# Performance work log

Measured on AMD Instinct MI355X. Metric: run time of the kernel, lower is better.

Reference implementation:

```python
import jax, jax.numpy as jnp
import numpy as np

TAU = 20.0        # LIFNeuron default tau
THRESHOLD = 1.0   # LIFNeuron default threshold
RESET = 0.0       # LIFNeuron default reset
DT = 1.0          # SpikingNeuralNetwork dt
ALPHA = DT / TAU

B, T, I, H, O = 256, 128, 512, 1024, 512


def setup_inputs() -> dict:
    key = jax.random.key(0)
    ks = jax.random.split(key, 6)
    def w(k, shape, fan_in):
        return (jax.random.normal(k, shape, jnp.float32) / np.sqrt(fan_in)).astype(jnp.float32)
    return {
        "x":  jax.random.normal(ks[0], (B, T, I), jnp.float32),
        "We": w(ks[1], (I, H), I), "be": jnp.zeros((H,), jnp.float32),
        "W1": w(ks[2], (H, H), H), "b1": jnp.zeros((H,), jnp.float32),
        "W2": w(ks[3], (H, H), H), "b2": jnp.zeros((H,), jnp.float32),
        "Wo": w(ks[4], (H, O), H), "bo": jnp.zeros((O,), jnp.float32),
    }


def _lif(v, inp):
    # v += (-v + inp) * dt/tau; spike = (v >= thr); v = v*(1-spike) + reset*spike
    v = v + (inp - v) * ALPHA
    spike = (v >= THRESHOLD).astype(v.dtype)
    v = v * (1.0 - spike) + RESET * spike
    return v, spike


def reference(x, We, be, W1, b1, W2, b2, Wo, bo):
    b, t, _ = x.shape
    h_dim = We.shape[1]
    o_dim = Wo.shape[1]

    def step(carry, xt):
        v1, v2, vo = carry
        h = jax.nn.relu(xt @ We + be)          # [B, H]
        v1, s1 = _lif(v1, h)                   # neuron 0 (only 2 of 3 neurons used: zip truncation)
        h = s1 @ W1 + b1
        v2, s2 = _lif(v2, h)                   # neuron 1
        h = s2 @ W2 + b2                       # last hidden layer: no neuron applied before output_layer
        vo, so = _lif(vo, h @ Wo + bo)         # output neuron
        return (v1, v2, vo), (s1, s2, so)

    init = (jnp.zeros((b, h_dim), x.dtype),
            jnp.zeros((b, h_dim), x.dtype),
            jnp.zeros((b, o_dim), x.dtype))
    _, (S1, S2, SO) = jax.lax.scan(step, init, jnp.swapaxes(x, 0, 1))  # time-major scan
    # output_spike at last timestep + full (detached) spike history, stacked over time
    return SO[-1], S1, S2, SO
```

## Files before the change

kernel.cpp:

```cpp
#include <hip/hip_runtime.h>
#include <cstdint>
#include <cstddef>

#define B_ 256
#define T_ 128
#define I_ 512
#define H_ 1024
#define O_ 512
static constexpr float ALPHA = 1.0f / 20.0f;
static constexpr float THR   = 1.0f;
static constexpr float S12   = 0.000244140625f;

typedef _Float16 f16;
typedef __attribute__((ext_vector_type(8))) _Float16 f16x8;
typedef __attribute__((ext_vector_type(4))) float f32x4;

template<bool PERM_X, bool RELU>
__global__ __launch_bounds__(256)
void gemm128(const float* __restrict__ A, const float* __restrict__ Bw,
             const float* __restrict__ bias, float* __restrict__ C,
             int M, int N, int K) {
    constexpr int BM = 128, BN = 128, BK = 16, TM = 8, TN = 8;
    __shared__ float As[BK][BM];
    __shared__ float Bs[BK][BN + 4];

    const int tid = threadIdx.x;
    const int ntile = N / BN;
    const int bx = blockIdx.x % ntile;
    const int by = blockIdx.x / ntile;
    const int row0 = by * BM, col0 = bx * BN;
    const int tx = tid & 15;
    const int ty = tid >> 4;

    float acc[TM][TN] = {};

    for (int k0 = 0; k0 < K; k0 += BK) {
#pragma unroll
        for (int p = 0; p < 2; ++p) {
            int f = tid + p * 256;
            int r  = f >> 2;
            int kc = (f & 3) << 2;
            int m = row0 + r;
            const float* arow;
            if (PERM_X) {
                int t = m >> 8;
                int b = m & 255;
                arow = A + (size_t)(b * T_ + t) * K;
            } else {
                arow = A + (size_t)m * K;
            }
            float4 v = *reinterpret_cast<const float4*>(arow + k0 + kc);
            As[kc + 0][r] = v.x;
            As[kc + 1][r] = v.y;
            As[kc + 2][r] = v.z;
            As[kc + 3][r] = v.w;
        }
#pragma unroll
        for (int p = 0; p < 2; ++p) {
            int f = tid + p * 256;
            int r  = f >> 5;
            int nc = (f & 31) << 2;
            float4 v = *reinterpret_cast<const float4*>(Bw + (size_t)(k0 + r) * N + col0 + nc);
            *reinterpret_cast<float4*>(&Bs[r][nc]) = v;
        }
        __syncthreads();

#pragma unroll
        for (int k = 0; k < BK; ++k) {
            float a[TM], b[TN];
#pragma unroll
            for (int i = 0; i < TM; ++i) a[i] = As[k][ty * TM + i];
#pragma unroll
            for (int j = 0; j < TN; ++j) b[j] = Bs[k][tx * TN + j];
#pragma unroll
            for (int i = 0; i < TM; ++i)
#pragma unroll
                for (int j = 0; j < TN; ++j)
                    acc[i][j] += a[i] * b[j];
        }
        __syncthreads();
    }

#pragma unroll
    for (int i = 0; i < TM; ++i) {
        size_t m = (size_t)(row0 + ty * TM + i);
#pragma unroll
        for (int jj = 0; jj < TN; jj += 4) {
            int n = col0 + tx * TN + jj;
            float4 c4;
            float c0 = acc[i][jj + 0] + bias[n + 0];
            float c1 = acc[i][jj + 1] + bias[n + 1];
            float c2 = acc[i][jj + 2] + bias[n + 2];
            float c3 = acc[i][jj + 3] + bias[n + 3];
            if (RELU) {
                c0 = fmaxf(c0, 0.f); c1 = fmaxf(c1, 0.f);
                c2 = fmaxf(c2, 0.f); c3 = fmaxf(c3, 0.f);
            }
            c4.x = c0; c4.y = c1; c4.z = c2; c4.w = c3;
            *reinterpret_cast<float4*>(C + m * N + n) = c4;
        }
    }
}

__device__ inline void gload_lds16(const void* gsrc, void* ldsdst) {
    __builtin_amdgcn_global_load_lds(
        (const __attribute__((address_space(1))) unsigned int*)gsrc,
        (__attribute__((address_space(3))) unsigned int*)ldsdst, 16, 0, 0);
}

template<bool SPLITX, bool PERM, bool RELU, bool WRITE_LAST>
__global__ __launch_bounds__(256, 2)
void gemm_lif(const float* __restrict__ A,
              const f16* __restrict__ Bhi,
              const f16* __restrict__ Blo,
              const float* __restrict__ bias,
              float* __restrict__ S,
              float* __restrict__ last_out,
              int N, int K) {
    constexpr int BK = 32;
    __shared__ __align__(16) char smem[128 * 132 * 4];
    f16* Ah = (f16*)smem;
    f16* Bh = Ah + 4096;
    f16* Bl = Bh + 4096;
    f16* Al = Bl + 4096;
    float (*Cs)[132] = (float (*)[132])smem;

    const int tid  = threadIdx.x;
    const int lane = tid & 63;
    const int w    = tid >> 6;
    const int wr   = w >> 1, wc = w & 1;
    const int ntile = N >> 7;
    const int bx = blockIdx.x % ntile;
    const int b  = blockIdx.x / ntile;
    const int col0 = bx << 7;

    f32x4 acc0[4][4], acc1[4][4];
#pragma unroll
    for (int mi = 0; mi < 4; ++mi)
#pragma unroll
        for (int ni = 0; ni < 4; ++ni) {
            acc0[mi][ni] = {0.f, 0.f, 0.f, 0.f};
            acc1[mi][ni] = {0.f, 0.f, 0.f, 0.f};
        }

    for (int k0 = 0; k0 < K; k0 += BK) {
#pragma unroll
        for (int p = 0; p < 2; ++p) {
            int chunk = w * 2 + p;
            int r  = chunk * 16 + (lane >> 2);
            int kq = lane & 3;
            size_t off = (size_t)(col0 + r) * K + k0 + kq * 8;
            gload_lds16(Bhi + off, &Bh[chunk * 512]);
            gload_lds16(Blo + off, &Bl[chunk * 512]);
        }
#pragma unroll
        for (int p = 0; p < 4; ++p) {
            int c = tid + p * 256;
            int r = c >> 3;
            int q = c & 7;
            const float* arow;
            if (PERM) arow = A + (size_t)(b * T_ + r) * K;
            else      arow = A + (size_t)(r * B_ + b) * K;
            float4 v = *reinterpret_cast<const float4*>(arow + k0 + q * 4);
            union { f16 h[4]; uint2 u; } hi;
            hi.h[0] = (f16)v.x; hi.h[1] = (f16)v.y;
            hi.h[2] = (f16)v.z; hi.h[3] = (f16)v.w;
            *reinterpret_cast<uint2*>(&Ah[r * BK + q * 4]) = hi.u;
            if (SPLITX) {
                union { f16 h[4]; uint2 u; } lo;
                lo.h[0] = (f16)((v.x - (float)hi.h[0]) * 4096.0f);
                lo.h[1] = (f16)((v.y - (float)hi.h[1]) * 4096.0f);
                lo.h[2] = (f16)((v.z - (float)hi.h[2]) * 4096.0f);
                lo.h[3] = (f16)((v.w - (float)hi.h[3]) * 4096.0f);
                *reinterpret_cast<uint2*>(&Al[r * BK + q * 4]) = lo.u;
            }
        }
        __syncthreads();

        f16x8 ahi[4], alo[4];
#pragma unroll
        for (int mi = 0; mi < 4; ++mi) {
            int ar = (wr * 64 + mi * 16 + (lane & 15)) * BK + (lane >> 4) * 8;
            ahi[mi] = *reinterpret_cast<const f16x8*>(&Ah[ar]);
            if (SPLITX) alo[mi] = *reinterpret_cast<const f16x8*>(&Al[ar]);
        }
#pragma unroll
        for (int ni = 0; ni < 4; ++ni) {
            int br = (wc * 64 + ni * 16 + (lane & 15)) * BK + (lane >> 4) * 8;
            f16x8 bh = *reinterpret_cast<const f16x8*>(&Bh[br]);
            f16x8 bl = *reinterpret_cast<const f16x8*>(&Bl[br]);
#pragma unroll
            for (int mi = 0; mi < 4; ++mi) {
                acc0[mi][ni] = __builtin_amdgcn_mfma_f32_16x16x32_f16(
                    ahi[mi], bh, acc0[mi][ni], 0, 0, 0);
                acc1[mi][ni] = __builtin_amdgcn_mfma_f32_16x16x32_f16(
                    ahi[mi], bl, acc1[mi][ni], 0, 0, 0);
                if (SPLITX)
                    acc1[mi][ni] = __builtin_amdgcn_mfma_f32_16x16x32_f16(
                        alo[mi], bh, acc1[mi][ni], 0, 0, 0);
            }
        }
        __syncthreads();
    }

#pragma unroll
    for (int ni = 0; ni < 4; ++ni) {
        int col = wc * 64 + ni * 16 + (lane & 15);
        float bv = bias[col0 + col];
#pragma unroll
        for (int mi = 0; mi < 4; ++mi) {
            int rowb = wr * 64 + mi * 16 + ((lane >> 4) << 2);
#pragma unroll
            for (int r = 0; r < 4; ++r) {
                float cv = acc0[mi][ni][r] + S12 * acc1[mi][ni][r] + bv;
                if (RELU) cv = fmaxf(cv, 0.f);
                Cs[rowb + r][col] = cv;
            }
        }
    }
    __syncthreads();

    if (tid < 128) {
        float* Sp = S + (size_t)b * N + col0 + tid;
        const size_t tstride = (size_t)B_ * N;
        float v = 0.f, s = 0.f;
#pragma unroll 4
        for (int t = 0; t < T_; ++t) {
            float in = Cs[t][tid];
            v = v + (in - v) * ALPHA;
            bool sp = (v >= THR);
            s = sp ? 1.0f : 0.0f;
            Sp[(size_t)t * tstride] = s;
            v = sp ? 0.0f : v;
        }
        if (WRITE_LAST) last_out[(size_t)b * N + col0 + tid] = s;
    }
}

__global__ __launch_bounds__(256)
void lif_scan(float* __restrict__ buf, int BH, float* __restrict__ last_out) {
    int j = blockIdx.x * 256 + threadIdx.x;
    if (j >= BH) return;
    float v = 0.f;
    float last = 0.f;
    for (int t = 0; t < T_; ++t) {
        size_t idx = (size_t)t * BH + j;
        float in = buf[idx];
        v = v + (in - v) * ALPHA;
        bool sp = (v >= THR);
        last = sp ? 1.0f : 0.0f;
        buf[idx] = last;
        v = sp ? 0.0f : v;
    }
    if (last_out) last_out[j] = last;
}

__global__ __launch_bounds__(256)
void make_wf2(const float* __restrict__ W2, const float* __restrict__ Wo,
              float* __restrict__ Wf) {
    __shared__ float w2s[64][33];
    __shared__ float wos[64][68];
    const int tid = threadIdx.x;
    const int ht = blockIdx.x >> 3, ot = blockIdx.x & 7;
    const int h0 = ht * 32, o0 = ot * 64;
    const int th = tid >> 3;
    const int to = tid & 7;

    double acc[8] = {0, 0, 0, 0, 0, 0, 0, 0};

    for (int k0 = 0; k0 < H_; k0 += 64) {
#pragma unroll
        for (int p = 0; p < 2; ++p) {
            int f = tid + p * 256;
            int i = f >> 4;
            int j4 = (f & 15) << 2;
            float4 v = *reinterpret_cast<const float4*>(
                W2 + (size_t)(h0 + i) * H_ + k0 + j4);
            w2s[j4 + 0][i] = v.x; w2s[j4 + 1][i] = v.y;
            w2s[j4 + 2][i] = v.z; w2s[j4 + 3][i] = v.w;
        }
#pragma unroll
        for (int p = 0; p < 4; ++p) {
            int f = tid + p * 256;
            int r = f >> 4;
            int c4 = (f & 15) << 2;
            float4 v = *reinterpret_cast<const float4*>(
                Wo + (size_t)(k0 + r) * O_ + o0 + c4);
            wos[r][c4 + 0] = v.x; wos[r][c4 + 1] = v.y;
            wos[r][c4 + 2] = v.z; wos[r][c4 + 3] = v.w;
        }
        __syncthreads();

#pragma unroll 8
        for (int k = 0; k < 64; ++k) {
            double a = (double)w2s[k][th];
#pragma unroll
            for (int j = 0; j < 8; ++j)
                acc[j] += a * (double)wos[k][to * 8 + j];
        }
        __syncthreads();
    }
#pragma unroll
    for (int j = 0; j < 8; ++j)
        Wf[(size_t)(h0 + th) * O_ + o0 + to * 8 + j] = (float)acc[j];
}

__global__ __launch_bounds__(256)
void make_bf(const float* __restrict__ Wo, const float* __restrict__ b2,
             const float* __restrict__ bo, float* __restrict__ bf) {
    int o = blockIdx.x * 256 + threadIdx.x;
    if (o >= O_) return;
    double acc = (double)bo[o];
    for (int h = 0; h < H_; ++h)
        acc += (double)b2[h] * (double)Wo[(size_t)h * O_ + o];
    bf[o] = (float)acc;
}

__global__ __launch_bounds__(256)
void split_w16(const float* __restrict__ W, f16* __restrict__ hi,
               f16* __restrict__ lo, int K, int N) {
    int idx = blockIdx.x * 256 + threadIdx.x;
    if (idx >= K * N) return;
    int n = idx / K;
    int k = idx - n * K;
    float wv = W[(size_t)k * N + n];
    f16 h0 = (f16)wv;
    float r = (wv - (float)h0) * 4096.0f;
    f16 h1 = (f16)r;
    hi[idx] = h0; lo[idx] = h1;
}

extern "C" void kernel_launch(void* const* d_in, const int* in_sizes, int n_in,
                              void* d_out, int out_size, void* d_ws, size_t ws_size,
                              hipStream_t stream) {
    const float* x  = (const float*)d_in[0];
    const float* We = (const float*)d_in[1];
    const float* be = (const float*)d_in[2];
    const float* W1 = (const float*)d_in[3];
    const float* b1 = (const float*)d_in[4];
    const float* W2 = (const float*)d_in[5];
    const float* b2 = (const float*)d_in[6];
    const float* Wo = (const float*)d_in[7];
    const float* bo = (const float*)d_in[8];

    float* out = (float*)d_out;
    float* so_last = out;
    float* S1 = out + (size_t)B_ * O_;
    float* S2 = S1 + (size_t)T_ * B_ * H_;
    float* SO = S2 + (size_t)T_ * B_ * H_;

    const int TB = T_ * B_;
    dim3 blk(256);

    const size_t sz_we  = (size_t)I_ * H_ * 2;
    const size_t sz_w1  = (size_t)H_ * H_ * 2;
    const size_t sz_wf  = (size_t)H_ * O_ * 2;
    const size_t off_weh = 0;
    const size_t off_wel = off_weh + sz_we;
    const size_t off_w1h = off_wel + sz_we;
    const size_t off_w1l = off_w1h + sz_w1;
    const size_t off_wf32 = off_w1l + sz_w1;
    const size_t off_bf   = off_wf32 + (size_t)H_ * O_ * 4;
    const size_t off_wfh  = off_bf + (size_t)O_ * 4;
    const size_t off_wfl  = off_wfh + sz_wf;
    const size_t need     = off_wfl + sz_wf;

    if (ws_size >= need) {
        char* ws = (char*)d_ws;
        f16*   weh = (f16*)(ws + off_weh);
        f16*   wel = (f16*)(ws + off_wel);
        f16*   w1h = (f16*)(ws + off_w1h);
        f16*   w1l = (f16*)(ws + off_w1l);
        float* Wf  = (float*)(ws + off_wf32);
        float* bf  = (float*)(ws + off_bf);
        f16*   wfh = (f16*)(ws + off_wfh);
        f16*   wfl = (f16*)(ws + off_wfl);

        split_w16<<<dim3((I_ * H_ + 255) / 256), blk, 0, stream>>>(We, weh, wel, I_, H_);
        split_w16<<<dim3((H_ * H_ + 255) / 256), blk, 0, stream>>>(W1, w1h, w1l, H_, H_);
        make_wf2<<<dim3(256), blk, 0, stream>>>(W2, Wo, Wf);
        make_bf<<<dim3(2), blk, 0, stream>>>(Wo, b2, bo, bf);
        split_w16<<<dim3((H_ * O_ + 255) / 256), blk, 0, stream>>>(Wf, wfh, wfl, H_, O_);

        gemm_lif<true, true, true, false><<<dim3(B_ * (H_ / 128)), blk, 0, stream>>>(
            x, weh, wel, be, S1, nullptr, H_, I_);

        gemm_lif<false, false, false, false><<<dim3(B_ * (H_ / 128)), blk, 0, stream>>>(
            S1, w1h, w1l, b1, S2, nullptr, H_, H_);

        gemm_lif<false, false, false, true><<<dim3(B_ * (O_ / 128)), blk, 0, stream>>>(
            S2, wfh, wfl, bf, SO, so_last, O_, H_);
    } else {
        float* Wf = (float*)d_ws;
        float* bf = Wf + (size_t)H_ * O_;
        gemm128<true, true><<<dim3((TB / 128) * (H_ / 128)), blk, 0, stream>>>(
            x, We, be, S1, TB, H_, I_);
        lif_scan<<<dim3((B_ * H_ + 255) / 256), blk, 0, stream>>>(S1, B_ * H_, nullptr);
        gemm128<false, false><<<dim3((TB / 128) * (H_ / 128)), blk, 0, stream>>>(
            S1, W1, b1, S2, TB, H_, H_);
        lif_scan<<<dim3((B_ * H_ + 255) / 256), blk, 0, stream>>>(S2, B_ * H_, nullptr);
        make_wf2<<<dim3(256), blk, 0, stream>>>(W2, Wo, Wf);
        make_bf<<<dim3(2), blk, 0, stream>>>(Wo, b2, bo, bf);
        gemm128<false, false><<<dim3((TB / 128) * (O_ / 128)), blk, 0, stream>>>(
            S2, Wf, bf, SO, TB, O_, H_);
        lif_scan<<<dim3((B_ * O_ + 255) / 256), blk, 0, stream>>>(SO, B_ * O_, so_last);
    }
}
```

Before: 643.4 us.

## Use 512-thread blocks, halve LDS epilogue with two-phase LIF scan, reorder grid

The fused GEMM+LIF kernel now runs with 512 threads (8 waves in a 2x4 layout), so each wave holds half the accumulators. The C staging buffer is cut to 64 rows, and the epilogue writes and scans the two halves of the time axis in turn. Together these lower LDS and register use so more blocks can be resident per CU. The block index now puts the batch in the low bits, so consecutive blocks share a weight column tile, which may improve L2 reuse of weights. The cost is extra barriers, and only 128 threads are busy during the serial LIF scan while the other waves sit idle.

After: 699.8 us. 8.8% more time.

```diff
diff --git a/kernel.cpp b/kernel.cpp
--- a/kernel.cpp
+++ b/kernel.cpp
@@ -109,7 +109,7 @@
 }
 
 template<bool SPLITX, bool PERM, bool RELU, bool WRITE_LAST>
-__global__ __launch_bounds__(256, 2)
+__global__ __launch_bounds__(512, 4)
 void gemm_lif(const float* __restrict__ A,
               const f16* __restrict__ Bhi,
               const f16* __restrict__ Blo,
@@ -118,7 +118,7 @@
               float* __restrict__ last_out,
               int N, int K) {
     constexpr int BK = 32;
-    __shared__ __align__(16) char smem[128 * 132 * 4];
+    __shared__ __align__(16) char smem[64 * 132 * 4];
     f16* Ah = (f16*)smem;
     f16* Bh = Ah + 4096;
     f16* Bl = Bh + 4096;
@@ -128,34 +128,32 @@
     const int tid  = threadIdx.x;
     const int lane = tid & 63;
     const int w    = tid >> 6;
-    const int wr   = w >> 1, wc = w & 1;
-    const int ntile = N >> 7;
-    const int bx = blockIdx.x % ntile;
-    const int b  = blockIdx.x / ntile;
+    const int wr   = w >> 2;
+    const int wc   = w & 3;
+    const int b    = blockIdx.x & 255;
+    const int bx   = blockIdx.x >> 8;
     const int col0 = bx << 7;
 
-    f32x4 acc0[4][4], acc1[4][4];
+    f32x4 acc0[4][2], acc1[4][2];
 #pragma unroll
     for (int mi = 0; mi < 4; ++mi)
 #pragma unroll
-        for (int ni = 0; ni < 4; ++ni) {
+        for (int ni = 0; ni < 2; ++ni) {
             acc0[mi][ni] = {0.f, 0.f, 0.f, 0.f};
             acc1[mi][ni] = {0.f, 0.f, 0.f, 0.f};
         }
 
     for (int k0 = 0; k0 < K; k0 += BK) {
-#pragma unroll
-        for (int p = 0; p < 2; ++p) {
-            int chunk = w * 2 + p;
-            int r  = chunk * 16 + (lane >> 2);
+        {
+            int r  = w * 16 + (lane >> 2);
             int kq = lane & 3;
             size_t off = (size_t)(col0 + r) * K + k0 + kq * 8;
-            gload_lds16(Bhi + off, &Bh[chunk * 512]);
-            gload_lds16(Blo + off, &Bl[chunk * 512]);
-        }
-#pragma unroll
-        for (int p = 0; p < 4; ++p) {
-            int c = tid + p * 256;
+            gload_lds16(Bhi + off, &Bh[w * 512]);
+            gload_lds16(Blo + off, &Bl[w * 512]);
+        }
+#pragma unroll
+        for (int p = 0; p < 2; ++p) {
+            int c = tid + p * 512;
             int r = c >> 3;
             int q = c & 7;
             const float* arow;
@@ -185,8 +183,8 @@
             if (SPLITX) alo[mi] = *reinterpret_cast<const f16x8*>(&Al[ar]);
         }
 #pragma unroll
-        for (int ni = 0; ni < 4; ++ni) {
-            int br = (wc * 64 + ni * 16 + (lane & 15)) * BK + (lane >> 4) * 8;
+        for (int ni = 0; ni < 2; ++ni) {
+            int br = (wc * 32 + ni * 16 + (lane & 15)) * BK + (lane >> 4) * 8;
             f16x8 bh = *reinterpret_cast<const f16x8*>(&Bh[br]);
             f16x8 bl = *reinterpret_cast<const f16x8*>(&Bl[br]);
 #pragma unroll
@@ -203,30 +201,62 @@
         __syncthreads();
     }
 
-#pragma unroll
-    for (int ni = 0; ni < 4; ++ni) {
-        int col = wc * 64 + ni * 16 + (lane & 15);
-        float bv = bias[col0 + col];
-#pragma unroll
-        for (int mi = 0; mi < 4; ++mi) {
-            int rowb = wr * 64 + mi * 16 + ((lane >> 4) << 2);
-#pragma unroll
-            for (int r = 0; r < 4; ++r) {
-                float cv = acc0[mi][ni][r] + S12 * acc1[mi][ni][r] + bv;
-                if (RELU) cv = fmaxf(cv, 0.f);
-                Cs[rowb + r][col] = cv;
+    float v = 0.f, s = 0.f;
+    float* Sp = S + (size_t)b * N + col0 + (tid & 127);
+    const size_t tstride = (size_t)B_ * N;
+
+    if (wr == 0) {
+#pragma unroll
+        for (int ni = 0; ni < 2; ++ni) {
+            int col = wc * 32 + ni * 16 + (lane & 15);
+            float bv = bias[col0 + col];
+#pragma unroll
+            for (int mi = 0; mi < 4; ++mi) {
+                int rowb = mi * 16 + ((lane >> 4) << 2);
+#pragma unroll
+                for (int r = 0; r < 4; ++r) {
+                    float cv = acc0[mi][ni][r] + S12 * acc1[mi][ni][r] + bv;
+                    if (RELU) cv = fmaxf(cv, 0.f);
+                    Cs[rowb + r][col] = cv;
+                }
             }
         }
     }
     __syncthreads();
-
     if (tid < 128) {
-        float* Sp = S + (size_t)b * N + col0 + tid;
-        const size_t tstride = (size_t)B_ * N;
-        float v = 0.f, s = 0.f;
 #pragma unroll 4
-        for (int t = 0; t < T_; ++t) {
+        for (int t = 0; t < 64; ++t) {
             float in = Cs[t][tid];
+            v = v + (in - v) * ALPHA;
+            bool sp = (v >= THR);
+            s = sp ? 1.0f : 0.0f;
+            Sp[(size_t)t * tstride] = s;
+            v = sp ? 0.0f : v;
+        }
+    }
+    __syncthreads();
+    if (wr == 1) {
+#pragma unroll
+        for (int ni = 0; ni < 2; ++ni) {
+            int col = wc * 32 + ni * 16 + (lane & 15);
+            float bv = bias[col0 + col];
+#pragma unroll
+            for (int mi = 0; mi < 4; ++mi) {
+                int rowb = mi * 16 + ((lane >> 4) << 2);
+#pragma unroll
+                for (int r = 0; r < 4; ++r) {
+                    float cv = acc0[mi][ni][r] + S12 * acc1[mi][ni][r] + bv;
+                    if (RELU) cv = fmaxf(cv, 0.f);
+                    Cs[rowb + r][col] = cv;
+                }
+            }
+        }
+    }
+    __syncthreads();
+    if (tid < 128) {
+#pragma unroll 4
+        for (int t = 64; t < 128; ++t) {
+            float in = Cs[t - 64][tid];
             v = v + (in - v) * ALPHA;
             bool sp = (v >= THR);
             s = sp ? 1.0f : 0.0f;
@@ -351,6 +381,7 @@
 
     const int TB = T_ * B_;
     dim3 blk(256);
+    dim3 blk512(512);
 
     const size_t sz_we  = (size_t)I_ * H_ * 2;
     const size_t sz_w1  = (size_t)H_ * H_ * 2;
@@ -382,13 +413,13 @@
         make_bf<<<dim3(2), blk, 0, stream>>>(Wo, b2, bo, bf);
         split_w16<<<dim3((H_ * O_ + 255) / 256), blk, 0, stream>>>(Wf, wfh, wfl, H_, O_);
 
-        gemm_lif<true, true, true, false><<<dim3(B_ * (H_ / 128)), blk, 0, stream>>>(
+        gemm_lif<true, true, true, false><<<dim3((H_ / 128) * B_), blk512, 0, stream>>>(
             x, weh, wel, be, S1, nullptr, H_, I_);
 
-        gemm_lif<false, false, false, false><<<dim3(B_ * (H_ / 128)), blk, 0, stream>>>(
+        gemm_lif<false, false, false, false><<<dim3((H_ / 128) * B_), blk512, 0, stream>>>(
             S1, w1h, w1l, b1, S2, nullptr, H_, H_);
 
-        gemm_lif<false, false, false, true><<<dim3(B_ * (O_ / 128)), blk, 0, stream>>>(
+        gemm_lif<false, false, false, true><<<dim3((O_ / 128) * B_), blk512, 0, stream>>>(
             S2, wfh, wfl, bf, SO, so_last, O_, H_);
     } else {
         float* Wf = (float*)d_ws;
```

## Double-buffer LDS tiles in fused GEMM+LIF and split epilogue into halves

Applied to the files above, without the earlier changes.

Adds double buffering to the gemm_lif main loop. The next K-tile's B halves are issued via global_load_lds and its A rows are prefetched into registers while MFMAs run on the current tile, leaving one barrier per iteration instead of two. To keep the LDS footprint bounded, the epilogue now stages the 128x128 result in two 64-row halves, with the LIF time scan run over each half in turn. This costs more LDS for the two buffers, extra barriers in the epilogue, and more register pressure from the prefetched float4s, which may hurt occupancy at launch_bounds(256,2).

Result: no change. 644.3 us (+0.1%).

```diff
diff --git a/kernel.cpp b/kernel.cpp
--- a/kernel.cpp
+++ b/kernel.cpp
@@ -118,11 +118,13 @@
               float* __restrict__ last_out,
               int N, int K) {
     constexpr int BK = 32;
-    __shared__ __align__(16) char smem[128 * 132 * 4];
-    f16* Ah = (f16*)smem;
-    f16* Bh = Ah + 4096;
-    f16* Bl = Bh + 4096;
-    f16* Al = Bl + 4096;
+    constexpr int NBUF = SPLITX ? 4 : 3;
+    constexpr int BUFSTR = NBUF * 4096;
+    constexpr size_t SMEM = (2 * BUFSTR * 2 > 64 * 132 * 4)
+                                ? (size_t)(2 * BUFSTR * 2)
+                                : (size_t)(64 * 132 * 4);
+    __shared__ __align__(16) char smem[SMEM];
+    f16* sm = (f16*)smem;
     float (*Cs)[132] = (float (*)[132])smem;
 
     const int tid  = threadIdx.x;
@@ -143,90 +145,187 @@
             acc1[mi][ni] = {0.f, 0.f, 0.f, 0.f};
         }
 
-    for (int k0 = 0; k0 < K; k0 += BK) {
+    {
+        f16* Ah0 = sm;
+        f16* Bh0 = sm + 4096;
+        f16* Bl0 = sm + 8192;
+        f16* Al0 = sm + 12288;
 #pragma unroll
         for (int p = 0; p < 2; ++p) {
             int chunk = w * 2 + p;
             int r  = chunk * 16 + (lane >> 2);
             int kq = lane & 3;
-            size_t off = (size_t)(col0 + r) * K + k0 + kq * 8;
-            gload_lds16(Bhi + off, &Bh[chunk * 512]);
-            gload_lds16(Blo + off, &Bl[chunk * 512]);
+            size_t off = (size_t)(col0 + r) * K + kq * 8;
+            gload_lds16(Bhi + off, Bh0 + chunk * 512);
+            gload_lds16(Blo + off, Bl0 + chunk * 512);
         }
 #pragma unroll
         for (int p = 0; p < 4; ++p) {
             int c = tid + p * 256;
             int r = c >> 3;
             int q = c & 7;
-            const float* arow;
-            if (PERM) arow = A + (size_t)(b * T_ + r) * K;
-            else      arow = A + (size_t)(r * B_ + b) * K;
-            float4 v = *reinterpret_cast<const float4*>(arow + k0 + q * 4);
+            const float* arow = PERM ? A + (size_t)(b * T_ + r) * K
+                                     : A + (size_t)(r * B_ + b) * K;
+            float4 v = *reinterpret_cast<const float4*>(arow + q * 4);
             union { f16 h[4]; uint2 u; } hi;
             hi.h[0] = (f16)v.x; hi.h[1] = (f16)v.y;
             hi.h[2] = (f16)v.z; hi.h[3] = (f16)v.w;
-            *reinterpret_cast<uint2*>(&Ah[r * BK + q * 4]) = hi.u;
+            *reinterpret_cast<uint2*>(&Ah0[r * BK + q * 4]) = hi.u;
             if (SPLITX) {
                 union { f16 h[4]; uint2 u; } lo;
                 lo.h[0] = (f16)((v.x - (float)hi.h[0]) * 4096.0f);
                 lo.h[1] = (f16)((v.y - (float)hi.h[1]) * 4096.0f);
                 lo.h[2] = (f16)((v.z - (float)hi.h[2]) * 4096.0f);
                 lo.h[3] = (f16)((v.w - (float)hi.h[3]) * 4096.0f);
-                *reinterpret_cast<uint2*>(&Al[r * BK + q * 4]) = lo.u;
+                *reinterpret_cast<uint2*>(&Al0[r * BK + q * 4]) = lo.u;
+            }
+        }
+    }
+    __syncthreads();
+
+    const int NIT = K / BK;
+    for (int it = 0; it < NIT; ++it) {
+        const int cur = it & 1, nxt = cur ^ 1;
+        const bool more = (it + 1 < NIT);
+        const int k0n = (it + 1) * BK;
+
+        f16* Ah_c = sm + cur * BUFSTR;
+        f16* Bh_c = Ah_c + 4096;
+        f16* Bl_c = Ah_c + 8192;
+        f16* Al_c = Ah_c + 12288;
+        f16* Ah_n = sm + nxt * BUFSTR;
+        f16* Bh_n = Ah_n + 4096;
+        f16* Bl_n = Ah_n + 8192;
+        f16* Al_n = Ah_n + 12288;
+
+        float4 a4[4];
+        if (more) {
+#pragma unroll
+            for (int p = 0; p < 2; ++p) {
+                int chunk = w * 2 + p;
+                int r  = chunk * 16 + (lane >> 2);
+                int kq = lane & 3;
+                size_t off = (size_t)(col0 + r) * K + k0n + kq * 8;
+                gload_lds16(Bhi + off, Bh_n + chunk * 512);
+                gload_lds16(Blo + off, Bl_n + chunk * 512);
+            }
+#pragma unroll
+            for (int p = 0; p < 4; ++p) {
+                int c = tid + p * 256;
+                int r = c >> 3;
+                int q = c & 7;
+                const float* arow = PERM ? A + (size_t)(b * T_ + r) * K
+                                         : A + (size_t)(r * B_ + b) * K;
+                a4[p] = *reinterpret_cast<const float4*>(arow + k0n + q * 4);
+            }
+        }
+
+        {
+            f16x8 ahi[4], alo[4];
+#pragma unroll
+            for (int mi = 0; mi < 4; ++mi) {
+                int ar = (wr * 64 + mi * 16 + (lane & 15)) * BK + (lane >> 4) * 8;
+                ahi[mi] = *reinterpret_cast<const f16x8*>(&Ah_c[ar]);
+                if (SPLITX) alo[mi] = *reinterpret_cast<const f16x8*>(&Al_c[ar]);
+            }
+#pragma unroll
+            for (int ni = 0; ni < 4; ++ni) {
+                int br = (wc * 64 + ni * 16 + (lane & 15)) * BK + (lane >> 4) * 8;
+                f16x8 bh = *reinterpret_cast<const f16x8*>(&Bh_c[br]);
+                f16x8 bl = *reinterpret_cast<const f16x8*>(&Bl_c[br]);
+#pragma unroll
+                for (int mi = 0; mi < 4; ++mi) {
+                    acc0[mi][ni] = __builtin_amdgcn_mfma_f32_16x16x32_f16(
+                        ahi[mi], bh, acc0[mi][ni], 0, 0, 0);
+                    acc1[mi][ni] = __builtin_amdgcn_mfma_f32_16x16x32_f16(
+                        ahi[mi], bl, acc1[mi][ni], 0, 0, 0);
+                    if (SPLITX)
+                        acc1[mi][ni] = __builtin_amdgcn_mfma_f32_16x16x32_f16(
+                            alo[mi], bh, acc1[mi][ni], 0, 0, 0);
+                }
+            }
+        }
+
+        if (more) {
+#pragma unroll
+            for (int p = 0; p < 4; ++p) {
+                int c = tid + p * 256;
+                int r = c >> 3;
+                int q = c & 7;
+                float4 v = a4[p];
+                union { f16 h[4]; uint2 u; } hi;
+                hi.h[0] = (f16)v.x; hi.h[1] = (f16)v.y;
+                hi.h[2] = (f16)v.z; hi.h[3] = (f16)v.w;
+                *reinterpret_cast<uint2*>(&Ah_n[r * BK + q * 4]) = hi.u;
+                if (SPLITX) {
+                    union { f16 h[4]; uint2 u; } lo;
+                    lo.h[0] = (f16)((v.x - (float)hi.h[0]) * 4096.0f);
+                    lo.h[1] = (f16)((v.y - (float)hi.h[1]) * 4096.0f);
+                    lo.h[2] = (f16)((v.z - (float)hi.h[2]) * 4096.0f);
+                    lo.h[3] = (f16)((v.w - (float)hi.h[3]) * 4096.0f);
+                    *reinterpret_cast<uint2*>(&Al_n[r * BK + q * 4]) = lo.u;
+                }
             }
         }
         __syncthreads();
-
-        f16x8 ahi[4], alo[4];
-#pragma unroll
-        for (int mi = 0; mi < 4; ++mi) {
-            int ar = (wr * 64 + mi * 16 + (lane & 15)) * BK + (lane >> 4) * 8;
-            ahi[mi] = *reinterpret_cast<const f16x8*>(&Ah[ar]);
-            if (SPLITX) alo[mi] = *reinterpret_cast<const f16x8*>(&Al[ar]);
-        }
+    }
+
+    float v = 0.f, s = 0.f;
+    float* Sp = S + (size_t)b * N + col0 + (tid & 127);
+    const size_t tstride = (size_t)B_ * N;
+
+    if (wr == 0) {
 #pragma unroll
         for (int ni = 0; ni < 4; ++ni) {
-            int br = (wc * 64 + ni * 16 + (lane & 15)) * BK + (lane >> 4) * 8;
-            f16x8 bh = *reinterpret_cast<const f16x8*>(&Bh[br]);
-            f16x8 bl = *reinterpret_cast<const f16x8*>(&Bl[br]);
+            int col = wc * 64 + ni * 16 + (lane & 15);
+            float bv = bias[col0 + col];
 #pragma unroll
             for (int mi = 0; mi < 4; ++mi) {
-                acc0[mi][ni] = __builtin_amdgcn_mfma_f32_16x16x32_f16(
-                    ahi[mi], bh, acc0[mi][ni], 0, 0, 0);
-                acc1[mi][ni] = __builtin_amdgcn_mfma_f32_16x16x32_f16(
-                    ahi[mi], bl, acc1[mi][ni], 0, 0, 0);
-                if (SPLITX)
-                    acc1[mi][ni] = __builtin_amdgcn_mfma_f32_16x16x32_f16(
-                        alo[mi], bh, acc1[mi][ni], 0, 0, 0);
-            }
-        }
-        __syncthreads();
-    }
-
-#pragma unroll
-    for (int ni = 0; ni < 4; ++ni) {
-        int col = wc * 64 + ni * 16 + (lane & 15);
-        float bv = bias[col0 + col];
-#pragma unroll
-        for (int mi = 0; mi < 4; ++mi) {
-            int rowb = wr * 64 + mi * 16 + ((lane >> 4) << 2);
-#pragma unroll
-            for (int r = 0; r < 4; ++r) {
-                float cv = acc0[mi][ni][r] + S12 * acc1[mi][ni][r] + bv;
-                if (RELU) cv = fmaxf(cv, 0.f);
-                Cs[rowb + r][col] = cv;
+                int rowb = mi * 16 + ((lane >> 4) << 2);
+#pragma unroll
+                for (int r = 0; r < 4; ++r) {
+                    float cv = acc0[mi][ni][r] + S12 * acc1[mi][ni][r] + bv;
+                    if (RELU) cv = fmaxf(cv, 0.f);
+                    Cs[rowb + r][col] = cv;
+                }
             }
         }
     }
     __syncthreads();
-
     if (tid < 128) {
-        float* Sp = S + (size_t)b * N + col0 + tid;
-        const size_t tstride = (size_t)B_ * N;
-        float v = 0.f, s = 0.f;
 #pragma unroll 4
-        for (int t = 0; t < T_; ++t) {
+        for (int t = 0; t < 64; ++t) {
             float in = Cs[t][tid];
+            v = v + (in - v) * ALPHA;
+            bool sp = (v >= THR);
+            s = sp ? 1.0f : 0.0f;
+            Sp[(size_t)t * tstride] = s;
+            v = sp ? 0.0f : v;
+        }
+    }
+    __syncthreads();
+    if (wr == 1) {
+#pragma unroll
+        for (int ni = 0; ni < 4; ++ni) {
+            int col = wc * 64 + ni * 16 + (lane & 15);
+            float bv = bias[col0 + col];
+#pragma unroll
+            for (int mi = 0; mi < 4; ++mi) {
+                int rowb = mi * 16 + ((lane >> 4) << 2);
+#pragma unroll
+                for (int r = 0; r < 4; ++r) {
+                    float cv = acc0[mi][ni][r] + S12 * acc1[mi][ni][r] + bv;
+                    if (RELU) cv = fmaxf(cv, 0.f);
+                    Cs[rowb + r][col] = cv;
+                }
+            }
+        }
+    }
+    __syncthreads();
+    if (tid < 128) {
+#pragma unroll 4
+        for (int t = 64; t < 128; ++t) {
+            float in = Cs[t - 64][tid];
             v = v + (in - v) * ALPHA;
             bool sp = (v >= THR);
             s = sp ? 1.0f : 0.0f;
```
